# Performance work log

Measured on AMD Instinct MI355X. Metric: run time of the kernel, lower is better.

Reference implementation:

```python
import jax, jax.numpy as jnp
import numpy as np

EPS = 1e-6

def _linear_params(key, d_in, d_out):
    w = jax.random.normal(key, (d_in, d_out), dtype=jnp.float32) * np.sqrt(2.0 / (d_in + d_out))
    b = jnp.zeros((d_out,), dtype=jnp.float32)
    return w, b

def setup_inputs() -> dict:
    key = jax.random.key(0)
    ks = jax.random.split(key, 8)
    B, S, D = 4, 2048, 1024
    x = jax.random.normal(ks[0], (B, S, D), dtype=jnp.float32)
    wq, bq = _linear_params(ks[1], D, D)
    wk, bk = _linear_params(ks[2], D, D)
    wv, bv = _linear_params(ks[3], D, D)
    wo, bo = _linear_params(ks[4], D, D)
    w1, b1 = _linear_params(ks[5], D, D)
    w2, b2 = _linear_params(ks[6], D, D)
    g1 = jnp.ones((D,), jnp.float32); be1 = jnp.zeros((D,), jnp.float32)
    g2 = jnp.ones((D,), jnp.float32); be2 = jnp.zeros((D,), jnp.float32)
    return {"x": x, "wq": wq, "bq": bq, "wk": wk, "bk": bk, "wv": wv, "bv": bv,
            "wo": wo, "bo": bo, "w1": w1, "b1": b1, "w2": w2, "b2": b2,
            "g1": g1, "be1": be1, "g2": g2, "be2": be2}

def _layernorm(x, gamma, beta):
    mean = jnp.mean(x, axis=-1, keepdims=True)
    # torch .std() default is unbiased (ddof=1); eps added to std (not var)
    std = jnp.std(x, axis=-1, keepdims=True, ddof=1)
    return gamma * (x - mean) / (std + EPS) + beta

def _attention(x, wq, bq, wk, bk, wv, bv, wo, bo):
    S = x.shape[-2]
    q = x @ wq + bq  # [B,S,D]
    k = x @ wk + bk
    v = x @ wv + bv
    scores = jnp.einsum('bsd,btd->bst', q, k) / jnp.sqrt(jnp.asarray(S, jnp.float32))
    causal = jnp.tril(jnp.ones((S, S), dtype=bool))  # keep lower triangle incl. diag
    scores = jnp.where(causal, scores, -jnp.inf)
    attn = jax.nn.softmax(scores, axis=-1)
    out = jnp.einsum('bst,btd->bsd', attn, v)
    return out @ wo + bo

def reference(x, wq, bq, wk, bk, wv, bv, wo, bo, w1, b1, w2, b2, g1, be1, g2, be2):
    h = _attention(_layernorm(x, g1, be1), wq, bq, wk, bk, wv, bv, wo, bo) + x
    m = _layernorm(h, g2, be2)
    m = jnp.maximum(m @ w1 + b1, 0.0) @ w2 + b2
    return m + h
```

## Files before the change

### kernel.cpp

```cpp
#include <hip/hip_runtime.h>
#include <math.h>

#define BB 4
#define SS 2048
#define DD 1024
#define MM (BB*SS)
#define SD ((size_t)SS*DD)
#define MD ((size_t)MM*DD)
#define PPB ((size_t)2162688)

#define WT_OFF (3*MD + 4*PPB)
#define ZP_OFF (WT_OFF + 6*(size_t)DD*DD)
#define REQ_WS ((ZP_OFF + 16) * 2)

constexpr float LN_EPS = 1e-6f;

typedef __attribute__((ext_vector_type(8))) __bf16 bf16x8;
typedef __attribute__((ext_vector_type(4))) float f32x4;

__device__ __forceinline__ unsigned short f2bfbits(float f){
    unsigned u = __float_as_uint(f);
    u += 0x7FFFu + ((u >> 16) & 1u);
    return (unsigned short)(u >> 16);
}
__device__ __forceinline__ int rowWidth(int s){ return ((s >> 6) + 1) << 6; }
__device__ __forceinline__ size_t rowOff(int s){
    int g = s >> 6;
    return (size_t)4096 * (size_t)((g * (g + 1)) >> 1) + (size_t)(s & 63) * (size_t)((g + 1) << 6);
}
__device__ __forceinline__ void gl_lds(const unsigned short* g, unsigned short* l){
    __builtin_amdgcn_global_load_lds(
        (const __attribute__((address_space(1))) unsigned int*)g,
        (__attribute__((address_space(3))) unsigned int*)l, 16, 0, 0);
}

__device__ __forceinline__ int3 xcd_swz(){
    const int gx = gridDim.x, gy = gridDim.y, gz = gridDim.z;
    const int n = gx * gy * gz;
    int lin = blockIdx.x + gx * (blockIdx.y + gy * blockIdx.z);
    const int cpx = n >> 3;
    lin = (lin & 7) * cpx + (lin >> 3);
    int3 r;
    r.x = lin % gx; lin /= gx;
    r.y = lin % gy;
    r.z = lin / gy;
    return r;
}

__global__ __launch_bounds__(256)
void sentinel_kernel(float* __restrict__ out, const float val){
    out[(size_t)blockIdx.x * 256 + threadIdx.x] = val;
}

struct WPack { const float* w[6]; unsigned short* o[6]; unsigned short* zp; };
__global__ __launch_bounds__(256)
void wtrans(WPack wp)
{
    __shared__ float Ts[64][65];
    const float* W = wp.w[blockIdx.z];
    unsigned short* WT = wp.o[blockIdx.z];
    const int r0 = blockIdx.y*64, c0 = blockIdx.x*64;
    const int tid = threadIdx.x;
    if (blockIdx.x == 0 && blockIdx.y == 0 && blockIdx.z == 0 && tid < 16) wp.zp[tid] = 0;
    #pragma unroll
    for (int i = 0; i < 16; ++i){
        int lin = tid + i*256;
        int r = lin >> 6, c = lin & 63;
        Ts[r][c] = W[(size_t)(r0+r)*DD + c0+c];
    }
    __syncthreads();
    #pragma unroll
    for (int i = 0; i < 16; ++i){
        int lin = tid + i*256;
        int r = lin >> 6, c = lin & 63;
        WT[(size_t)(c0+r)*DD + r0+c] = f2bfbits(Ts[c][r]);
    }
}

__global__ __launch_bounds__(256)
void ln_f32(const float* __restrict__ x, const float* __restrict__ gamma,
            const float* __restrict__ beta, unsigned short* __restrict__ out)
{
    __shared__ float red[4];
    const int row = blockIdx.x;
    const int tid = threadIdx.x;
    float4 xv = ((const float4*)(x + (size_t)row*DD))[tid];
    float v[4] = {xv.x, xv.y, xv.z, xv.w};
    float s = v[0]+v[1]+v[2]+v[3];
    #pragma unroll
    for (int off = 32; off > 0; off >>= 1) s += __shfl_down(s, off, 64);
    if ((tid & 63) == 0) red[tid >> 6] = s;
    __syncthreads();
    const float mean = (red[0]+red[1]+red[2]+red[3]) * (1.0f/DD);
    __syncthreads();
    float q = 0.f;
    #pragma unroll
    for (int i = 0; i < 4; ++i){ float d = v[i]-mean; q += d*d; }
    #pragma unroll
    for (int off = 32; off > 0; off >>= 1) q += __shfl_down(q, off, 64);
    if ((tid & 63) == 0) red[tid >> 6] = q;
    __syncthreads();
    const float var = (red[0]+red[1]+red[2]+red[3]) * (1.0f/(DD-1));
    const float inv = 1.0f/(sqrtf(var) + LN_EPS);
    float4 g4 = ((const float4*)gamma)[tid];
    float4 b4 = ((const float4*)beta)[tid];
    ushort4 o;
    o.x = f2bfbits(g4.x*(v[0]-mean)*inv + b4.x);
    o.y = f2bfbits(g4.y*(v[1]-mean)*inv + b4.y);
    o.z = f2bfbits(g4.z*(v[2]-mean)*inv + b4.z);
    o.w = f2bfbits(g4.w*(v[3]-mean)*inv + b4.w);
    ((ushort4*)(out + (size_t)row*DD))[tid] = o;
}

template<bool PACKED_A>
__device__ __forceinline__ void gemm_loop8(
    const unsigned short* const ga[4], const unsigned short* const gb[2],
    const int* pw, const unsigned short* zpad,
    const int NT, unsigned short* S, f32x4 acc[4][4],
    const int wave, const int lane)
{
    unsigned short* A0 = S;
    unsigned short* A1 = S + 16384;
    unsigned short* A2 = S + 32768;
    unsigned short* B0 = S + 49152;
    unsigned short* B1 = S + 57344;
    unsigned short* B2 = S + 65536;

    const int quad = lane >> 4, l15 = lane & 15;
    const int wr = (wave >> 1) * 64;
    const int wc = (wave & 1) * 64;

    auto stageA = [&](unsigned short* buf, int koff){
        #pragma unroll
        for (int c = 0; c < 4; ++c){
            const unsigned short* gp = ga[c] + koff;
            if constexpr (PACKED_A) { if (koff >= pw[c]) gp = zpad; }
            gl_lds(gp, &buf[(wave*4+c)*512]);
        }
    };
    auto stageB = [&](unsigned short* buf, int koff){
        #pragma unroll
        for (int c = 0; c < 2; ++c) gl_lds(gb[c] + koff, &buf[(wave*2+c)*512]);
    };

    stageA(A0, 0);  stageB(B0, 0);
    stageA(A1, 64); stageB(B1, 64);
    asm volatile("s_waitcnt vmcnt(6)" ::: "memory");
    __builtin_amdgcn_s_barrier();

    for (int t = 0; t < NT; ++t){
        const int kn = (t + 2) << 6;
        const bool more2 = (t + 2 < NT);
        #pragma unroll
        for (int kk = 0; kk < 2; ++kk){
            bf16x8 af[4], bfr[4];
            #pragma unroll
            for (int u = 0; u < 4; ++u){
                const int ra = wr + u*16 + l15, rb = wc + u*16 + l15, gi = kk*4 + quad;
                af[u]  = *(const bf16x8*)&A0[ra*64 + (((gi + ra) & 7) << 3)];
                bfr[u] = *(const bf16x8*)&B0[rb*64 + (((gi + rb) & 7) << 3)];
            }
            if (kk == 0 && more2){
                stageA(A2, kn); stageB(B2, kn);
            }
            __builtin_amdgcn_s_barrier();
            asm volatile("s_waitcnt lgkmcnt(0)" ::: "memory");
            __builtin_amdgcn_sched_barrier(0);
            __builtin_amdgcn_s_setprio(1);
            #pragma unroll
            for (int i = 0; i < 4; ++i)
                #pragma unroll
                for (int j = 0; j < 4; ++j)
                    acc[i][j] = __builtin_amdgcn_mfma_f32_16x16x32_bf16(af[i], bfr[j], acc[i][j], 0, 0, 0);
            __builtin_amdgcn_s_setprio(0);
            if (kk == 1){
                if (more2) asm volatile("s_waitcnt vmcnt(6)" ::: "memory");
                else       asm volatile("s_waitcnt vmcnt(0)" ::: "memory");
            }
            __builtin_amdgcn_s_barrier();
        }
        unsigned short* ta = A0; A0 = A1; A1 = A2; A2 = ta;
        unsigned short* tb = B0; B0 = B1; B1 = B2; B2 = tb;
    }
}

__device__ __forceinline__ void mk_ga(const unsigned short* base, size_t ld, int r0,
                                      int wave, int lane, const unsigned short* ga[4]){
    #pragma unroll
    for (int c = 0; c < 4; ++c){
        const int mr = (wave*4 + c)*8 + (lane >> 3);
        const int gk = ((lane & 7) - mr) & 7;
        ga[c] = base + (size_t)(r0 + mr)*ld + gk*8;
    }
}
__device__ __forceinline__ void mk_gb(const unsigned short* base, size_t ld, int r0,
                                      int wave, int lane, const unsigned short* gb[2]){
    #pragma unroll
    for (int c = 0; c < 2; ++c){
        const int mr = (wave*2 + c)*8 + (lane >> 3);
        const int gk = ((lane & 7) - mr) & 7;
        gb[c] = base + (size_t)(r0 + mr)*ld + gk*8;
    }
}

template<bool RELU, bool RES, bool OUTF, bool BIAS_M>
__global__ __launch_bounds__(512)
void gemm_mfma(const unsigned short* __restrict__ A, const unsigned short* __restrict__ B,
               const float* __restrict__ bias, const float* __restrict__ resF,
               unsigned short* __restrict__ outB, float* __restrict__ outF,
               const int N, const int K, const int lda, const int ldb)
{
    __shared__ unsigned short Smem[73728];
    const int3 b = xcd_swz();
    const int m0 = b.y*256, n0 = b.x*128;
    const int tid = threadIdx.x, lane = tid & 63, wave = tid >> 6;
    const unsigned short* ga[4]; const unsigned short* gb[2];
    mk_ga(A, lda, m0, wave, lane, ga);
    mk_gb(B, ldb, n0, wave, lane, gb);
    f32x4 acc[4][4] = {};
    gemm_loop8<false>(ga, gb, nullptr, nullptr, K >> 6, Smem, acc, wave, lane);

    const int quad = lane >> 4, l15 = lane & 15;
    const int wr = (wave >> 1) * 64, wc = (wave & 1) * 64;
    #pragma unroll
    for (int i = 0; i < 4; ++i){
        #pragma unroll
        for (int r = 0; r < 4; ++r){
            const int m = m0 + wr + i*16 + quad*4 + r;
            const float bm = BIAS_M ? bias[m] : 0.f;
            #pragma unroll
            for (int j = 0; j < 4; ++j){
                const int n = n0 + wc + j*16 + l15;
                float v = acc[i][j][r] + (BIAS_M ? bm : bias[n]);
                if constexpr (RELU) v = fmaxf(v, 0.f);
                if constexpr (RES) v += resF[(size_t)m*N + n];
                if constexpr (OUTF) outF[(size_t)m*N + n] = v;
                else outB[(size_t)m*N + n] = f2bfbits(v);
            }
        }
    }
}

__global__ __launch_bounds__(512)
void gemm_qk(const unsigned short* __restrict__ LN,
             const unsigned short* __restrict__ WqT, const unsigned short* __restrict__ WkT,
             const float* __restrict__ bq, const float* __restrict__ bk,
             unsigned short* __restrict__ Qw, unsigned short* __restrict__ Kw)
{
    __shared__ unsigned short Smem[73728];
    const int3 b = xcd_swz();
    const bool isK = (b.z != 0);
    const unsigned short* Bw = isK ? WkT : WqT;
    const float* bias = isK ? bk : bq;
    unsigned short* out = isK ? Kw : Qw;
    const int m0 = b.y*256, n0 = b.x*128;
    const int tid = threadIdx.x, lane = tid & 63, wave = tid >> 6;
    const unsigned short* ga[4]; const unsigned short* gb[2];
    mk_ga(LN, DD, m0, wave, lane, ga);
    mk_gb(Bw, DD, n0, wave, lane, gb);
    f32x4 acc[4][4] = {};
    gemm_loop8<false>(ga, gb, nullptr, nullptr, DD >> 6, Smem, acc, wave, lane);

    const int quad = lane >> 4, l15 = lane & 15;
    const int wr = (wave >> 1) * 64, wc = (wave & 1) * 64;
    #pragma unroll
    for (int i = 0; i < 4; ++i){
        #pragma unroll
        for (int r = 0; r < 4; ++r){
            const int m = m0 + wr + i*16 + quad*4 + r;
            #pragma unroll
            for (int j = 0; j < 4; ++j){
                const int n = n0 + wc + j*16 + l15;
                out[(size_t)m*DD + n] = f2bfbits(acc[i][j][r] + bias[n]);
            }
        }
    }
}

__global__ __launch_bounds__(512)
void scores_mfma(const unsigned short* __restrict__ Qb, const unsigned short* __restrict__ Kb,
                 unsigned short* __restrict__ Pb, const float scale)
{
    const int3 b = xcd_swz();
    const int s0 = b.y*256, t0 = b.x*128;
    if (t0 >= s0 + 256) return;
    const unsigned short* Q  = Qb + (size_t)b.z*SD;
    const unsigned short* Km = Kb + (size_t)b.z*SD;
    unsigned short* P        = Pb + (size_t)b.z*PPB;
    __shared__ unsigned short Smem[73728];
    const int tid = threadIdx.x, lane = tid & 63, wave = tid >> 6;
    const unsigned short* ga[4]; const unsigned short* gb[2];
    mk_ga(Q,  DD, s0, wave, lane, ga);
    mk_gb(Km, DD, t0, wave, lane, gb);
    f32x4 acc[4][4] = {};
    gemm_loop8<false>(ga, gb, nullptr, nullptr, DD >> 6, Smem, acc, wave, lane);

    const int quad = lane >> 4, l15 = lane & 15;
    const int wr = (wave >> 1) * 64, wc = (wave & 1) * 64;
    #pragma unroll
    for (int i = 0; i < 4; ++i){
        #pragma unroll
        for (int r = 0; r < 4; ++r){
            const int s = s0 + wr + i*16 + quad*4 + r;
            const int width = rowWidth(s);
            unsigned short* pr = P + rowOff(s);
            #pragma unroll
            for (int j = 0; j < 4; ++j){
                const int t = t0 + wc + j*16 + l15;
                if (t < width) pr[t] = f2bfbits(acc[i][j][r] * scale);
            }
        }
    }
}

__global__ __launch_bounds__(256)
void softmax_p(unsigned short* __restrict__ Pb)
{
    __shared__ float red[4];
    const int s = blockIdx.x;
    const int width = rowWidth(s);
    unsigned short* r = Pb + (size_t)blockIdx.y * PPB + rowOff(s);
    const int tid = threadIdx.x;
    float vals[8];
    float m = -1e30f;
    #pragma unroll
    for (int i = 0; i < 8; ++i){
        int t = tid + i*256;
        float v = -1e30f;
        if (t <= s) v = __uint_as_float(((unsigned)r[t]) << 16);
        vals[i] = v; m = fmaxf(m, v);
    }
    #pragma unroll
    for (int off = 32; off > 0; off >>= 1) m = fmaxf(m, __shfl_down(m, off, 64));
    if ((tid & 63) == 0) red[tid >> 6] = m;
    __syncthreads();
    const float M4 = fmaxf(fmaxf(red[0],red[1]), fmaxf(red[2],red[3]));
    __syncthreads();
    float ev[8]; float sum = 0.f;
    #pragma unroll
    for (int i = 0; i < 8; ++i){ ev[i] = __expf(vals[i] - M4); sum += ev[i]; }
    #pragma unroll
    for (int off = 32; off > 0; off >>= 1) sum += __shfl_down(sum, off, 64);
    if ((tid & 63) == 0) red[tid >> 6] = sum;
    __syncthreads();
    const float inv = 1.0f / (red[0]+red[1]+red[2]+red[3]);
    #pragma unroll
    for (int i = 0; i < 8; ++i){
        int t = tid + i*256;
        if (t < width) r[t] = f2bfbits(ev[i] * inv);
    }
}

__global__ __launch_bounds__(512)
void pv_mfma(const unsigned short* __restrict__ Pb, const unsigned short* __restrict__ VT,
             unsigned short* __restrict__ Cb, const unsigned short* __restrict__ zpad)
{
    const int3 b = xcd_swz();
    const int s0 = b.y*256, n0 = b.x*128;
    const unsigned short* P = Pb + (size_t)b.z*PPB;
    unsigned short* C       = Cb + (size_t)b.z*SD;
    const int bcol = b.z*SS;
    __shared__ unsigned short Smem[73728];
    const int tid = threadIdx.x, lane = tid & 63, wave = tid >> 6;
    const unsigned short* ga[4]; const unsigned short* gb[2]; int pw[4];
    #pragma unroll
    for (int c = 0; c < 4; ++c){
        const int mr = (wave*4 + c)*8 + (lane >> 3);
        const int gk = ((lane & 7) - mr) & 7;
        const int s = s0 + mr;
        pw[c] = rowWidth(s) - gk*8;
        ga[c] = P + rowOff(s) + gk*8;
    }
    #pragma unroll
    for (int c = 0; c < 2; ++c){
        const int mr = (wave*2 + c)*8 + (lane >> 3);
        const int gk = ((lane & 7) - mr) & 7;
        gb[c] = VT + (size_t)(n0 + mr)*MM + bcol + gk*8;
    }
    f32x4 acc[4][4] = {};
    const int NT = (s0 + 256) >> 6;
    gemm_loop8<true>(ga, gb, pw, zpad, NT, Smem, acc, wave, lane);

    const int quad = lane >> 4, l15 = lane & 15;
    const int wr = (wave >> 1) * 64, wc = (wave & 1) * 64;
    #pragma unroll
    for (int i = 0; i < 4; ++i){
        #pragma unroll
        for (int r = 0; r < 4; ++r){
            const int s = s0 + wr + i*16 + quad*4 + r;
            #pragma unroll
            for (int j = 0; j < 4; ++j){
                const int n = n0 + wc + j*16 + l15;
                C[(size_t)s*DD + n] = f2bfbits(acc[i][j][r]);
            }
        }
    }
}

extern "C" void kernel_launch(void* const* d_in, const int* in_sizes, int n_in,
                              void* d_out, int out_size, void* d_ws, size_t ws_size,
                              hipStream_t stream)
{
    (void)in_sizes; (void)n_in; (void)out_size;
    const float* x   = (const float*)d_in[0];
    const float* bq  = (const float*)d_in[2];
    const float* bk  = (const float*)d_in[4];
    const float* bv  = (const float*)d_in[6];
    const float* bo  = (const float*)d_in[8];
    const float* b1  = (const float*)d_in[10];
    const float* b2  = (const float*)d_in[12];
    const float* g1  = (const float*)d_in[13];
    const float* be1 = (const float*)d_in[14];
    const float* g2  = (const float*)d_in[15];
    const float* be2 = (const float*)d_in[16];
    float* outf = (float*)d_out;

    if (ws_size < (size_t)REQ_WS){
        sentinel_kernel<<<dim3((unsigned)(MD/256)), dim3(256), 0, stream>>>(outf, 1.0e9f);
        return;
    }

    unsigned short* wsb = (unsigned short*)d_ws;
    unsigned short* Qw  = wsb;
    unsigned short* Kw  = wsb + MD;
    unsigned short* VTw = wsb + 2*MD;
    unsigned short* Pw  = wsb + 3*MD;
    unsigned short* WT  = wsb + WT_OFF;
    unsigned short* ZP  = wsb + ZP_OFF;
    float*          Hf  = (float*)Kw;
    unsigned short* CTX = Qw;
    unsigned short* MIDw= Pw;
    unsigned short* LN  = (unsigned short*)d_out;

    WPack wp;
    static const int widx[6] = {1,3,5,7,9,11};
    for (int i = 0; i < 6; ++i){
        wp.w[i] = (const float*)d_in[widx[i]];
        wp.o[i] = WT + (size_t)i*DD*DD;
    }
    wp.zp = ZP;
    unsigned short* WqT = wp.o[0]; unsigned short* WkT = wp.o[1];
    unsigned short* WvT = wp.o[2]; unsigned short* WoT = wp.o[3];
    unsigned short* W1T = wp.o[4]; unsigned short* W2T = wp.o[5];

    const dim3 blk(256);
    const dim3 blk8(512);
    const float scale = 1.0f / sqrtf((float)SS);
    const dim3 gA8(DD/128, MM/256);
    const dim3 gVT8(MM/128, DD/256);

    wtrans<<<dim3(16,16,6), blk, 0, stream>>>(wp);
    ln_f32<<<dim3(MM), blk, 0, stream>>>(x, g1, be1, LN);
    gemm_qk<<<dim3(DD/128, MM/256, 2), blk8, 0, stream>>>(LN, WqT, WkT, bq, bk, Qw, Kw);
    gemm_mfma<false,false,false,true ><<<gVT8, blk8, 0, stream>>>(WvT, LN, bv, nullptr, VTw, nullptr, MM, DD, DD, DD);
    scores_mfma<<<dim3(SS/128, SS/256, BB), blk8, 0, stream>>>(Qw, Kw, Pw, scale);
    softmax_p<<<dim3(SS, BB), blk, 0, stream>>>(Pw);
    pv_mfma<<<dim3(DD/128, SS/256, BB), blk8, 0, stream>>>(Pw, VTw, CTX, ZP);
    gemm_mfma<false,true,true,false><<<gA8, blk8, 0, stream>>>(CTX, WoT, bo, x, nullptr, Hf, DD, DD, DD, DD);
    ln_f32<<<dim3(MM), blk, 0, stream>>>(Hf, g2, be2, LN);
    gemm_mfma<true,false,false,false><<<gA8, blk8, 0, stream>>>(LN, W1T, b1, nullptr, MIDw, nullptr, DD, DD, DD, DD);
    gemm_mfma<false,true,true,false><<<gA8, blk8, 0, stream>>>(MIDw, W2T, b2, Hf, nullptr, outf, DD, DD, DD, DD);
}
```

Baseline: 376.2 us.

## Switch GEMM main loop from triple-buffered to ping-pong double-buffered LDS

Replaces the three rotating LDS buffers with two statically declared A/B buffer pairs, used in an explicitly unrolled ping-pong schedule. The load for the next tile is issued between the two compute phases of the current tile, and each phase waits for all outstanding loads. Shared memory drops from 144KB to 96KB per block, which may allow more residency and removes the pointer rotation. In exchange there is less prefetch depth, since loads are only one stage ahead with a full vmcnt(0) wait. The tail also issues a redundant clamped load.

```diff
diff --git a/kernel.cpp b/kernel.cpp
--- a/kernel.cpp
+++ b/kernel.cpp
@@ -115,73 +115,65 @@
 template<bool PACKED_A>
 __device__ __forceinline__ void gemm_loop8(
     const unsigned short* const ga[4], const unsigned short* const gb[2],
-    const int* pw, const unsigned short* zpad,
-    const int NT, unsigned short* S, f32x4 acc[4][4],
-    const int wave, const int lane)
-{
-    unsigned short* A0 = S;
-    unsigned short* A1 = S + 16384;
-    unsigned short* A2 = S + 32768;
-    unsigned short* B0 = S + 49152;
-    unsigned short* B1 = S + 57344;
-    unsigned short* B2 = S + 65536;
-
+    const int* pw, const unsigned short* zpad, const int NT,
+    f32x4 acc[4][4], const int wave, const int lane,
+    unsigned short (&A_0)[16384], unsigned short (&B_0)[8192],
+    unsigned short (&A_1)[16384], unsigned short (&B_1)[8192])
+{
     const int quad = lane >> 4, l15 = lane & 15;
     const int wr = (wave >> 1) * 64;
     const int wc = (wave & 1) * 64;
 
-    auto stageA = [&](unsigned short* buf, int koff){
+    auto stage = [&](unsigned short (&Ab)[16384], unsigned short (&Bb)[8192], int koff){
         #pragma unroll
         for (int c = 0; c < 4; ++c){
             const unsigned short* gp = ga[c] + koff;
             if constexpr (PACKED_A) { if (koff >= pw[c]) gp = zpad; }
-            gl_lds(gp, &buf[(wave*4+c)*512]);
-        }
+            gl_lds(gp, &Ab[(wave*4+c)*512]);
+        }
+        #pragma unroll
+        for (int c = 0; c < 2; ++c) gl_lds(gb[c] + koff, &Bb[(wave*2+c)*512]);
     };
-    auto stageB = [&](unsigned short* buf, int koff){
-        #pragma unroll
-        for (int c = 0; c < 2; ++c) gl_lds(gb[c] + koff, &buf[(wave*2+c)*512]);
+    auto phase = [&](unsigned short (&Ab)[16384], unsigned short (&Bb)[8192],
+                     const int kk, const bool wait_vm){
+        bf16x8 af[4], bfr[4];
+        #pragma unroll
+        for (int u = 0; u < 4; ++u){
+            const int ra = wr + u*16 + l15, rb = wc + u*16 + l15, gi = kk*4 + quad;
+            af[u]  = *(const bf16x8*)&Ab[ra*64 + (((gi + ra) & 7) << 3)];
+            bfr[u] = *(const bf16x8*)&Bb[rb*64 + (((gi + rb) & 7) << 3)];
+        }
+        __builtin_amdgcn_s_barrier();
+        asm volatile("s_waitcnt lgkmcnt(0)" ::: "memory");
+        __builtin_amdgcn_sched_barrier(0);
+        __builtin_amdgcn_s_setprio(1);
+        #pragma unroll
+        for (int i = 0; i < 4; ++i)
+            #pragma unroll
+            for (int j = 0; j < 4; ++j)
+                acc[i][j] = __builtin_amdgcn_mfma_f32_16x16x32_bf16(af[i], bfr[j], acc[i][j], 0, 0, 0);
+        __builtin_amdgcn_s_setprio(0);
+        if (wait_vm)
+            asm volatile("s_waitcnt vmcnt(0)" ::: "memory");
+        __builtin_amdgcn_s_barrier();
     };
 
-    stageA(A0, 0);  stageB(B0, 0);
-    stageA(A1, 64); stageB(B1, 64);
+    stage(A_0, B_0, 0);
+    stage(A_1, B_1, 64);
     asm volatile("s_waitcnt vmcnt(6)" ::: "memory");
     __builtin_amdgcn_s_barrier();
 
-    for (int t = 0; t < NT; ++t){
-        const int kn = (t + 2) << 6;
-        const bool more2 = (t + 2 < NT);
-        #pragma unroll
-        for (int kk = 0; kk < 2; ++kk){
-            bf16x8 af[4], bfr[4];
-            #pragma unroll
-            for (int u = 0; u < 4; ++u){
-                const int ra = wr + u*16 + l15, rb = wc + u*16 + l15, gi = kk*4 + quad;
-                af[u]  = *(const bf16x8*)&A0[ra*64 + (((gi + ra) & 7) << 3)];
-                bfr[u] = *(const bf16x8*)&B0[rb*64 + (((gi + rb) & 7) << 3)];
-            }
-            if (kk == 0 && more2){
-                stageA(A2, kn); stageB(B2, kn);
-            }
-            __builtin_amdgcn_s_barrier();
-            asm volatile("s_waitcnt lgkmcnt(0)" ::: "memory");
-            __builtin_amdgcn_sched_barrier(0);
-            __builtin_amdgcn_s_setprio(1);
-            #pragma unroll
-            for (int i = 0; i < 4; ++i)
-                #pragma unroll
-                for (int j = 0; j < 4; ++j)
-                    acc[i][j] = __builtin_amdgcn_mfma_f32_16x16x32_bf16(af[i], bfr[j], acc[i][j], 0, 0, 0);
-            __builtin_amdgcn_s_setprio(0);
-            if (kk == 1){
-                if (more2) asm volatile("s_waitcnt vmcnt(6)" ::: "memory");
-                else       asm volatile("s_waitcnt vmcnt(0)" ::: "memory");
-            }
-            __builtin_amdgcn_s_barrier();
-        }
-        unsigned short* ta = A0; A0 = A1; A1 = A2; A2 = ta;
-        unsigned short* tb = B0; B0 = B1; B1 = B2; B2 = tb;
-    }
+    const int half = NT >> 1;
+    for (int i = 0; i < half; ++i){
+        if (i > 0) stage(A_1, B_1, (2*i + 1) << 6);
+        phase(A_0, B_0, 0, false);
+        phase(A_0, B_0, 1, true);
+        int kc = 2*i + 2; if (kc > NT - 1) kc = NT - 1;
+        stage(A_0, B_0, kc << 6);
+        phase(A_1, B_1, 0, false);
+        phase(A_1, B_1, 1, true);
+    }
+    asm volatile("s_waitcnt vmcnt(0)" ::: "memory");
 }
 
 __device__ __forceinline__ void mk_ga(const unsigned short* base, size_t ld, int r0,
@@ -202,6 +194,12 @@
         gb[c] = base + (size_t)(r0 + mr)*ld + gk*8;
     }
 }
+
+#define DECL_PAIRS \
+    __shared__ unsigned short A_0[16384]; \
+    __shared__ unsigned short B_0[8192];  \
+    __shared__ unsigned short A_1[16384]; \
+    __shared__ unsigned short B_1[8192];
 
 template<bool RELU, bool RES, bool OUTF, bool BIAS_M>
 __global__ __launch_bounds__(512)
@@ -210,7 +208,7 @@
                unsigned short* __restrict__ outB, float* __restrict__ outF,
                const int N, const int K, const int lda, const int ldb)
 {
-    __shared__ unsigned short Smem[73728];
+    DECL_PAIRS
     const int3 b = xcd_swz();
     const int m0 = b.y*256, n0 = b.x*128;
     const int tid = threadIdx.x, lane = tid & 63, wave = tid >> 6;
@@ -218,7 +216,7 @@
     mk_ga(A, lda, m0, wave, lane, ga);
     mk_gb(B, ldb, n0, wave, lane, gb);
     f32x4 acc[4][4] = {};
-    gemm_loop8<false>(ga, gb, nullptr, nullptr, K >> 6, Smem, acc, wave, lane);
+    gemm_loop8<false>(ga, gb, nullptr, nullptr, K >> 6, acc, wave, lane, A_0, B_0, A_1, B_1);
 
     const int quad = lane >> 4, l15 = lane & 15;
     const int wr = (wave >> 1) * 64, wc = (wave & 1) * 64;
@@ -247,7 +245,7 @@
              const float* __restrict__ bq, const float* __restrict__ bk,
              unsigned short* __restrict__ Qw, unsigned short* __restrict__ Kw)
 {
-    __shared__ unsigned short Smem[73728];
+    DECL_PAIRS
     const int3 b = xcd_swz();
     const bool isK = (b.z != 0);
     const unsigned short* Bw = isK ? WkT : WqT;
@@ -259,7 +257,7 @@
     mk_ga(LN, DD, m0, wave, lane, ga);
     mk_gb(Bw, DD, n0, wave, lane, gb);
     f32x4 acc[4][4] = {};
-    gemm_loop8<false>(ga, gb, nullptr, nullptr, DD >> 6, Smem, acc, wave, lane);
+    gemm_loop8<false>(ga, gb, nullptr, nullptr, DD >> 6, acc, wave, lane, A_0, B_0, A_1, B_1);
 
     const int quad = lane >> 4, l15 = lane & 15;
     const int wr = (wave >> 1) * 64, wc = (wave & 1) * 64;
@@ -287,13 +285,13 @@
     const unsigned short* Q  = Qb + (size_t)b.z*SD;
     const unsigned short* Km = Kb + (size_t)b.z*SD;
     unsigned short* P        = Pb + (size_t)b.z*PPB;
-    __shared__ unsigned short Smem[73728];
+    DECL_PAIRS
     const int tid = threadIdx.x, lane = tid & 63, wave = tid >> 6;
     const unsigned short* ga[4]; const unsigned short* gb[2];
     mk_ga(Q,  DD, s0, wave, lane, ga);
     mk_gb(Km, DD, t0, wave, lane, gb);
     f32x4 acc[4][4] = {};
-    gemm_loop8<false>(ga, gb, nullptr, nullptr, DD >> 6, Smem, acc, wave, lane);
+    gemm_loop8<false>(ga, gb, nullptr, nullptr, DD >> 6, acc, wave, lane, A_0, B_0, A_1, B_1);
 
     const int quad = lane >> 4, l15 = lane & 15;
     const int wr = (wave >> 1) * 64, wc = (wave & 1) * 64;
@@ -360,7 +358,7 @@
     const unsigned short* P = Pb + (size_t)b.z*PPB;
     unsigned short* C       = Cb + (size_t)b.z*SD;
     const int bcol = b.z*SS;
-    __shared__ unsigned short Smem[73728];
+    DECL_PAIRS
     const int tid = threadIdx.x, lane = tid & 63, wave = tid >> 6;
     const unsigned short* ga[4]; const unsigned short* gb[2]; int pw[4];
     #pragma unroll
@@ -379,7 +377,7 @@
     }
     f32x4 acc[4][4] = {};
     const int NT = (s0 + 256) >> 6;
-    gemm_loop8<true>(ga, gb, pw, zpad, NT, Smem, acc, wave, lane);
+    gemm_loop8<true>(ga, gb, pw, zpad, NT, acc, wave, lane, A_0, B_0, A_1, B_1);
 
     const int quad = lane >> 4, l15 = lane & 15;
     const int wr = (wave >> 1) * 64, wc = (wave & 1) * 64;
```

Result: slower. 394.9 us (+5.0%).
